# Performance work log

Measured on AMD Instinct MI355X. Metric: run time of the kernel, lower is better.

The kernel has to match this reference:

```python
import jax, jax.numpy as jnp
import numpy as np

D = 256; NH = 8; HD = 32; DFF = 1024; NL = 4; NPT = 4
SHAPES = [(100, 100), (50, 50), (25, 25), (13, 13)]
LEN_V = sum(h * w for h, w in SHAPES)  # 13294
BS = 16; LQ = 300


def _ln(x, g, b):
    m = jnp.mean(x, -1, keepdims=True)
    v = jnp.var(x, -1, keepdims=True)
    return (x - m) * jax.lax.rsqrt(v + 1e-5) * g + b


def _bilinear(v, loc, H, W):
    # v: [bs, nh, H*W, hd]; loc: [bs, Lq, nh, P, 2] normalized [0,1]
    # matches F.grid_sample(bilinear, align_corners=False, padding_mode='zeros')
    bs, Lq, nh, P, _ = loc.shape
    x = loc[..., 0] * W - 0.5
    y = loc[..., 1] * H - 0.5
    x0 = jnp.floor(x); y0 = jnp.floor(y)
    dx = x - x0; dy = y - y0
    x0 = x0.astype(jnp.int32); y0 = y0.astype(jnp.int32)
    out = jnp.zeros((bs, Lq, nh, P, v.shape[-1]), v.dtype)
    for ix, iy, w in ((x0, y0, (1 - dx) * (1 - dy)),
                      (x0 + 1, y0, dx * (1 - dy)),
                      (x0, y0 + 1, (1 - dx) * dy),
                      (x0 + 1, y0 + 1, dx * dy)):
        valid = (ix >= 0) & (ix < W) & (iy >= 0) & (iy < H)
        idx = jnp.clip(iy, 0, H - 1) * W + jnp.clip(ix, 0, W - 1)  # [bs,Lq,nh,P]
        idx = jnp.transpose(idx, (0, 2, 1, 3)).reshape(bs, nh, Lq * P, 1)
        g = jnp.take_along_axis(v, idx, axis=2).reshape(bs, nh, Lq, P, -1)
        g = jnp.transpose(g, (0, 2, 1, 3, 4))  # [bs,Lq,nh,P,hd]
        out = out + g * jnp.where(valid, w, jnp.zeros_like(w))[..., None]
    return out


def reference(tgt, reference_points, memory, Wq, bq, Wk, bk, Wv, bv, Wo, bo,
              Wvp, bvp, Wso, bso, Waw, baw, Wop, bop, W1, bf1, W2, bf2,
              ln1_g, ln1_b, ln2_g, ln2_b, ln3_g, ln3_b):
    bs, Lq, _ = tgt.shape
    # ---- self attention (query_pos_embed=None, attn_mask=None) ----
    qh = (tgt @ Wq + bq).reshape(bs, Lq, NH, HD)
    kh = (tgt @ Wk + bk).reshape(bs, Lq, NH, HD)
    vh = (tgt @ Wv + bv).reshape(bs, Lq, NH, HD)
    scores = jnp.einsum('bqhd,bkhd->bhqk', qh, kh) * np.float32(1.0 / np.sqrt(HD))
    attn = jax.nn.softmax(scores, -1)
    sa = jnp.einsum('bhqk,bkhd->bqhd', attn, vh).reshape(bs, Lq, D) @ Wo + bo
    t = _ln(tgt + sa, ln1_g, ln1_b)
    # ---- PP multi-scale deformable cross attention ----
    val = (memory @ Wvp + bvp).reshape(bs, LEN_V, NH, HD)
    val = jnp.transpose(val, (0, 2, 1, 3))  # [bs, nh, Lv, hd]
    off = (t @ Wso + bso).reshape(bs, Lq, NH, NL, NPT, 2)
    aw = jax.nn.softmax((t @ Waw + baw).reshape(bs, Lq, NH, NL * NPT), -1)
    aw = aw.reshape(bs, Lq, NH, NL, NPT)
    rp = reference_points  # [bs, Lq, NL, 4] -> (cx, cy, w, h) branch
    loc = rp[:, :, None, :, None, :2] + off / NPT * rp[:, :, None, :, None, 2:] * 0.5
    start = 0
    ca = jnp.zeros((bs, Lq, NH, HD), t.dtype)
    for l, (H, W) in enumerate(SHAPES):
        v_l = val[:, :, start:start + H * W]
        sampled = _bilinear(v_l, loc[:, :, :, l], H, W)  # [bs,Lq,nh,P,hd]
        ca = ca + jnp.einsum('bqhpd,bqhp->bqhd', sampled, aw[:, :, :, l])
        start += H * W
    ca = ca.reshape(bs, Lq, D) @ Wop + bop
    t = _ln(t + ca, ln2_g, ln2_b)
    # ---- FFN ----
    ff = jax.nn.relu(t @ W1 + bf1) @ W2 + bf2
    return _ln(t + ff, ln3_g, ln3_b)


def setup_inputs() -> dict:
    ks = iter(jax.random.split(jax.random.key(0), 64))
    inp = {}
    inp['tgt'] = jax.random.normal(next(ks), (BS, LQ, D), jnp.float32)
    inp['reference_points'] = jax.random.uniform(next(ks), (BS, LQ, NL, 4), jnp.float32)
    inp['memory'] = jax.random.normal(next(ks), (BS, LEN_V, D), jnp.float32)
    for name, sh in [('Wq', (D, D)), ('Wk', (D, D)), ('Wv', (D, D)), ('Wo', (D, D)),
                     ('Wvp', (D, D)), ('Wso', (D, NH * NL * NPT * 2)),
                     ('Waw', (D, NH * NL * NPT)), ('Wop', (D, D)),
                     ('W1', (D, DFF)), ('W2', (DFF, D))]:
        inp[name] = jax.random.normal(next(ks), sh, jnp.float32) * 0.02
    for name, dim in [('bq', D), ('bk', D), ('bv', D), ('bo', D), ('bvp', D),
                      ('bso', NH * NL * NPT * 2), ('baw', NH * NL * NPT),
                      ('bop', D), ('bf1', DFF), ('bf2', D)]:
        inp[name] = jnp.zeros((dim,), jnp.float32)
    for g, b in [('ln1_g', 'ln1_b'), ('ln2_g', 'ln2_b'), ('ln3_g', 'ln3_b')]:
        inp[g] = jnp.ones((D,), jnp.float32)
        inp[b] = jnp.zeros((D,), jnp.float32)
    return inp
```

## Files before the change

### kernel.cpp

```cpp
#include <hip/hip_runtime.h>
#include <hip/hip_bf16.h>
#include <cstddef>

#define D_    256
#define NH_   8
#define HD_   32
#define LQ_   300
#define BS_   16
#define LENV_ 13294
#define DFF_  1024
#define NROWS (BS_*LQ_)
#define VROWS (BS_*LENV_)

typedef __attribute__((ext_vector_type(8))) short short8;
typedef __attribute__((ext_vector_type(4))) float f32x4;
typedef unsigned int u32;

__device__ __forceinline__ short f2bf(float x) {
    unsigned u = __float_as_uint(x);
    u += 0x7fff + ((u >> 16) & 1);
    return (short)(u >> 16);
}
__device__ __forceinline__ unsigned pack_bf2(float lo, float hi) {
    return (unsigned)(unsigned short)f2bf(lo) | ((unsigned)(unsigned short)f2bf(hi) << 16);
}
__device__ __forceinline__ float bf2f(short s) {
    return __uint_as_float((unsigned)(unsigned short)s << 16);
}

__global__ __launch_bounds__(256) void prep_all(
    const float* __restrict__ Wq, const float* __restrict__ Wk,
    const float* __restrict__ Wv, const float* __restrict__ Wo,
    const float* __restrict__ Wvp, const float* __restrict__ Wso,
    const float* __restrict__ Waw, const float* __restrict__ Wop,
    const float* __restrict__ W1, const float* __restrict__ W2,
    const float* __restrict__ bqp, const float* __restrict__ bkp,
    const float* __restrict__ bvp, const float* __restrict__ bsop,
    const float* __restrict__ bawp,
    short* __restrict__ Wqkvt, short* __restrict__ Wot,
    short* __restrict__ Wvpt, short* __restrict__ Wsoawt,
    short* __restrict__ Wopt, short* __restrict__ W1t,
    short* __restrict__ W2t, float* __restrict__ bqkv,
    float* __restrict__ bsoaw)
{
    const int blk = blockIdx.x, tid = threadIdx.x;
    if (blk < 1792) {
        const int seg = blk >> 8;
        const int e = ((blk & 255) << 8) | tid;
        const int n = e >> 8, k = e & 255;
        const float* src; short* dst;
        switch (seg) {
            case 0: src = Wq;  dst = Wqkvt;          break;
            case 1: src = Wk;  dst = Wqkvt + 65536;  break;
            case 2: src = Wv;  dst = Wqkvt + 131072; break;
            case 3: src = Wo;  dst = Wot;            break;
            case 4: src = Wvp; dst = Wvpt;           break;
            case 5: src = Wso; dst = Wsoawt;         break;
            default: src = Wop; dst = Wopt;          break;
        }
        dst[e] = f2bf(src[(size_t)k * 256 + n]);
    } else if (blk < 1920) {
        const int e = ((blk - 1792) << 8) | tid;
        const int n = e >> 8, k = e & 255;
        Wsoawt[65536 + e] = f2bf(Waw[(size_t)k * 128 + n]);
    } else if (blk < 2048) {
        const int e = ((blk - 1920) << 8) | tid;
        Wsoawt[98304 + e] = 0;
    } else if (blk < 3072) {
        const int e = ((blk - 2048) << 8) | tid;
        const int n = e >> 8, k = e & 255;
        W1t[e] = f2bf(W1[(size_t)k * 1024 + n]);
    } else if (blk < 4096) {
        const int e = ((blk - 3072) << 8) | tid;
        const int n = e / 1024, k = e % 1024;
        W2t[e] = f2bf(W2[(size_t)k * 256 + n]);
    } else {
        const int e = ((blk - 4096) << 8) | tid;
        if (e < 768)
            bqkv[e] = (e < 256) ? bqp[e] : (e < 512) ? bkp[e - 256] : bvp[e - 512];
        else if (e < 1280) {
            const int f = e - 768;
            bsoaw[f] = (f < 256) ? bsop[f] : (f < 384) ? bawp[f - 256] : 0.f;
        }
    }
}

template<int ACT, int OUT_BF16, int STACKED>
__global__ __launch_bounds__(256) void mfma_gemm(
    const float* __restrict__ A, const short* __restrict__ Wt,
    const float* __restrict__ bias, void* __restrict__ Cout,
    int M, int N, int K)
{
    __shared__ short Alds[2][64 * 40];
    __shared__ short Blds[2][256 * 40];
    const int tid  = threadIdx.x;
    const int lane = tid & 63;
    const int wn   = tid >> 6;
    const int m0   = blockIdx.x * 64;
    const int nb   = blockIdx.y;
    const int srow = tid >> 2;
    const int schk = tid & 3;

    const int  arow = m0 + srow;
    const bool aok  = (arow < M);
    const float* aptr = &A[(size_t)(aok ? arow : 0) * K + schk * 8];
    const short* bptr = &Wt[(size_t)(nb * 256 + srow) * K + schk * 8];

    f32x4 acc[4][4] = {};
    float4 ra0, ra1;
    short8 rb0, rb1, rb2, rb3;

    ra0 = make_float4(0.f, 0.f, 0.f, 0.f); ra1 = ra0;
    if (aok) { ra0 = *(const float4*)(aptr); ra1 = *(const float4*)(aptr + 4); }
    rb0 = *(const short8*)(bptr);
    rb1 = *(const short8*)(bptr + (size_t)64 * K);
    rb2 = *(const short8*)(bptr + (size_t)128 * K);
    rb3 = *(const short8*)(bptr + (size_t)192 * K);
    {
        short8 s;
        s[0] = f2bf(ra0.x); s[1] = f2bf(ra0.y); s[2] = f2bf(ra0.z); s[3] = f2bf(ra0.w);
        s[4] = f2bf(ra1.x); s[5] = f2bf(ra1.y); s[6] = f2bf(ra1.z); s[7] = f2bf(ra1.w);
        *(short8*)&Alds[0][srow * 40 + schk * 8] = s;
        *(short8*)&Blds[0][(srow +   0) * 40 + schk * 8] = rb0;
        *(short8*)&Blds[0][(srow +  64) * 40 + schk * 8] = rb1;
        *(short8*)&Blds[0][(srow + 128) * 40 + schk * 8] = rb2;
        *(short8*)&Blds[0][(srow + 192) * 40 + schk * 8] = rb3;
    }
    __syncthreads();

    const int lg = lane >> 4;
    const int lr = lane & 15;
    int buf = 0;

    for (int k0 = 32; k0 < K; k0 += 32) {
        ra0 = make_float4(0.f, 0.f, 0.f, 0.f); ra1 = ra0;
        if (aok) { ra0 = *(const float4*)(aptr + k0); ra1 = *(const float4*)(aptr + k0 + 4); }
        rb0 = *(const short8*)(bptr + k0);
        rb1 = *(const short8*)(bptr + k0 + (size_t)64 * K);
        rb2 = *(const short8*)(bptr + k0 + (size_t)128 * K);
        rb3 = *(const short8*)(bptr + k0 + (size_t)192 * K);

        {
            short8 a[4], b[4];
            #pragma unroll
            for (int mr = 0; mr < 4; ++mr)
                a[mr] = *(const short8*)&Alds[buf][(mr * 16 + lr) * 40 + lg * 8];
            #pragma unroll
            for (int nr = 0; nr < 4; ++nr)
                b[nr] = *(const short8*)&Blds[buf][(wn * 64 + nr * 16 + lr) * 40 + lg * 8];
            #pragma unroll
            for (int mr = 0; mr < 4; ++mr)
                #pragma unroll
                for (int nr = 0; nr < 4; ++nr)
                    acc[mr][nr] = __builtin_amdgcn_mfma_f32_16x16x32_bf16(
                        a[mr], b[nr], acc[mr][nr], 0, 0, 0);
        }

        {
            short8 s;
            s[0] = f2bf(ra0.x); s[1] = f2bf(ra0.y); s[2] = f2bf(ra0.z); s[3] = f2bf(ra0.w);
            s[4] = f2bf(ra1.x); s[5] = f2bf(ra1.y); s[6] = f2bf(ra1.z); s[7] = f2bf(ra1.w);
            const int ob = buf ^ 1;
            *(short8*)&Alds[ob][srow * 40 + schk * 8] = s;
            *(short8*)&Blds[ob][(srow +   0) * 40 + schk * 8] = rb0;
            *(short8*)&Blds[ob][(srow +  64) * 40 + schk * 8] = rb1;
            *(short8*)&Blds[ob][(srow + 128) * 40 + schk * 8] = rb2;
            *(short8*)&Blds[ob][(srow + 192) * 40 + schk * 8] = rb3;
        }
        __syncthreads();
        buf ^= 1;
    }

    {
        short8 a[4], b[4];
        #pragma unroll
        for (int mr = 0; mr < 4; ++mr)
            a[mr] = *(const short8*)&Alds[buf][(mr * 16 + lr) * 40 + lg * 8];
        #pragma unroll
        for (int nr = 0; nr < 4; ++nr)
            b[nr] = *(const short8*)&Blds[buf][(wn * 64 + nr * 16 + lr) * 40 + lg * 8];
        #pragma unroll
        for (int mr = 0; mr < 4; ++mr)
            #pragma unroll
            for (int nr = 0; nr < 4; ++nr)
                acc[mr][nr] = __builtin_amdgcn_mfma_f32_16x16x32_bf16(
                    a[mr], b[nr], acc[mr][nr], 0, 0, 0);
    }

    if (STACKED) {
        float* Cb = (float*)Cout + (size_t)nb * M * 256;
        const float* bb = bias + nb * 256;
        #pragma unroll
        for (int mr = 0; mr < 4; ++mr)
            #pragma unroll
            for (int r = 0; r < 4; ++r) {
                const int row = m0 + mr * 16 + lg * 4 + r;
                if (row >= M) continue;
                #pragma unroll
                for (int nr = 0; nr < 4; ++nr) {
                    const int col = wn * 64 + nr * 16 + lr;
                    Cb[(size_t)row * 256 + col] = acc[mr][nr][r] + bb[col];
                }
            }
    } else {
        #pragma unroll
        for (int mr = 0; mr < 4; ++mr)
            #pragma unroll
            for (int r = 0; r < 4; ++r) {
                const int row = m0 + mr * 16 + lg * 4 + r;
                if (row >= M) continue;
                #pragma unroll
                for (int nr = 0; nr < 4; ++nr) {
                    const int col = nb * 256 + wn * 64 + nr * 16 + lr;
                    float v = acc[mr][nr][r] + bias[col];
                    if (ACT) v = fmaxf(v, 0.f);
                    if (OUT_BF16) ((short*)Cout)[(size_t)row * N + col] = f2bf(v);
                    else          ((float*)Cout)[(size_t)row * N + col] = v;
                }
            }
    }
}

__global__ __launch_bounds__(256, 2) void vp_gemm(
    const float* __restrict__ A, const short* __restrict__ Wt,
    const float* __restrict__ bias, short* __restrict__ C)
{
    __shared__ float Alds[2][32 * 256];
    __shared__ short Cst[32 * 256];
    const int tid  = threadIdx.x;
    const int lane = tid & 63;
    const int w    = tid >> 6;
    const int lr   = lane & 15;
    const int lg   = lane >> 4;

    short8 bf[4][8];
    #pragma unroll
    for (int nr = 0; nr < 4; ++nr) {
        const short* wp = &Wt[(size_t)(w * 64 + nr * 16 + lr) * 256 + lg * 8];
        #pragma unroll
        for (int kc = 0; kc < 8; ++kc)
            bf[nr][kc] = *(const short8*)(wp + kc * 32);
    }
    float bs[4];
    #pragma unroll
    for (int nr = 0; nr < 4; ++nr) bs[nr] = bias[w * 64 + nr * 16 + lr];

    const int NT = VROWS / 32;
    const int NB = 512;
    int t = blockIdx.x;
    int buf = 0;

    #define VP_STAGE(BUFI, TILE)                                               \
        {                                                                      \
            _Pragma("unroll")                                                  \
            for (int j = 0; j < 8; ++j) {                                      \
                const int r = w * 8 + j;                                       \
                const int grow = (TILE) * 32 + r;                              \
                const int c16 = ((((lane >> 1) ^ (r & 7)) << 1) | (lane & 1)); \
                const float* src = A + (size_t)grow * 256 + c16 * 4;           \
                __builtin_amdgcn_global_load_lds(                              \
                    (const __attribute__((address_space(1))) u32*)src,         \
                    (__attribute__((address_space(3))) u32*)&Alds[BUFI][r*256],\
                    16, 0, 0);                                                 \
            }                                                                  \
        }

    VP_STAGE(0, t);
    __syncthreads();

    while (true) {
        const int t2 = t + NB;
        if (t2 < NT) VP_STAGE(buf ^ 1, t2);

        f32x4 acc[2][4] = {};
        #pragma unroll
        for (int kc = 0; kc < 8; ++kc) {
            short8 a[2];
            #pragma unroll
            for (int mr = 0; mr < 2; ++mr) {
                const int row = mr * 16 + lr;
                const int c32 = (kc * 4 + lg) ^ (row & 7);
                const float* p = &Alds[buf][row * 256 + c32 * 8];
                float4 x = *(const float4*)(p);
                float4 y = *(const float4*)(p + 4);
                short8 s;
                s[0] = f2bf(x.x); s[1] = f2bf(x.y); s[2] = f2bf(x.z); s[3] = f2bf(x.w);
                s[4] = f2bf(y.x); s[5] = f2bf(y.y); s[6] = f2bf(y.z); s[7] = f2bf(y.w);
                a[mr] = s;
            }
            #pragma unroll
            for (int mr = 0; mr < 2; ++mr)
                #pragma unroll
                for (int nr = 0; nr < 4; ++nr)
                    acc[mr][nr] = __builtin_amdgcn_mfma_f32_16x16x32_bf16(
                        a[mr], bf[nr][kc], acc[mr][nr], 0, 0, 0);
        }

        #pragma unroll
        for (int mr = 0; mr < 2; ++mr)
            #pragma unroll
            for (int r4 = 0; r4 < 4; ++r4)
                #pragma unroll
                for (int nr = 0; nr < 4; ++nr)
                    Cst[(mr * 16 + lg * 4 + r4) * 256 + w * 64 + nr * 16 + lr] =
                        f2bf(acc[mr][nr][r4] + bs[nr]);
        __syncthreads();

        {
            const size_t base = (size_t)t * 32 * 256;
            #pragma unroll
            for (int j = 0; j < 4; ++j) {
                const int chunk = j * 256 + tid;
                *(short8*)&C[base + (size_t)chunk * 8] =
                    *(const short8*)&Cst[chunk * 8];
            }
        }
        __syncthreads();
        buf ^= 1;
        if (t2 >= NT) break;
        t = t2;
    }
    #undef VP_STAGE
}

__global__ __launch_bounds__(256) void attn_fused(
    const float* __restrict__ qh, const float* __restrict__ kh,
    const float* __restrict__ vh, float* __restrict__ sa)
{
    __shared__ short Klds[304 * 40];
    __shared__ short Vtlds[32 * 328];
    const int bh = blockIdx.x, b = bh / NH_, h = bh % NH_;
    const int tid = threadIdx.x;

    for (int idx = tid; idx < 304 * 4; idx += 256) {
        const int key = idx >> 2, dc = idx & 3;
        short8 s = {};
        if (key < LQ_) {
            const float* kp = &kh[((size_t)(b * LQ_ + key)) * D_ + h * HD_ + dc * 8];
            float4 a0 = *reinterpret_cast<const float4*>(kp);
            float4 a1 = *reinterpret_cast<const float4*>(kp + 4);
            s[0] = f2bf(a0.x); s[1] = f2bf(a0.y); s[2] = f2bf(a0.z); s[3] = f2bf(a0.w);
            s[4] = f2bf(a1.x); s[5] = f2bf(a1.y); s[6] = f2bf(a1.z); s[7] = f2bf(a1.w);
        }
        *reinterpret_cast<short8*>(&Klds[key * 40 + dc * 8]) = s;
    }
    for (int idx = tid; idx < LQ_ * 8; idx += 256) {
        const int key = idx >> 3, dc = idx & 7;
        const float4 v4 = *reinterpret_cast<const float4*>(
            &vh[((size_t)(b * LQ_ + key)) * D_ + h * HD_ + dc * 4]);
        Vtlds[(dc * 4 + 0) * 328 + key] = f2bf(v4.x);
        Vtlds[(dc * 4 + 1) * 328 + key] = f2bf(v4.y);
        Vtlds[(dc * 4 + 2) * 328 + key] = f2bf(v4.z);
        Vtlds[(dc * 4 + 3) * 328 + key] = f2bf(v4.w);
    }
    for (int idx = tid; idx < 32 * 20; idx += 256) {
        const int d = idx / 20, kk = idx % 20;
        Vtlds[d * 328 + 300 + kk] = 0;
    }
    __syncthreads();

    const int lane = tid & 63;
    const int wid  = tid >> 6;
    const int g    = lane >> 4;
    const int qc   = lane & 15;
    const int y    = blockIdx.y;
    const int qt_end = (y == 0) ? 10 : 19;

    for (int qt = y * 10 + wid; qt < qt_end; qt += 4) {
        const int q0 = qt * 16;
        short8 qf;
        {
            const int q = min(q0 + qc, LQ_ - 1);
            const float* qp = &qh[((size_t)(b * LQ_ + q)) * D_ + h * HD_ + g * 8];
            float4 a0 = *reinterpret_cast<const float4*>(qp);
            float4 a1 = *reinterpret_cast<const float4*>(qp + 4);
            const float sc = 0.17677669529663687f;
            qf[0] = f2bf(a0.x * sc); qf[1] = f2bf(a0.y * sc);
            qf[2] = f2bf(a0.z * sc); qf[3] = f2bf(a0.w * sc);
            qf[4] = f2bf(a1.x * sc); qf[5] = f2bf(a1.y * sc);
            qf[6] = f2bf(a1.z * sc); qf[7] = f2bf(a1.w * sc);
        }
        f32x4 s[19];
        #pragma unroll
        for (int kt = 0; kt < 19; ++kt) {
            short8 kf = *reinterpret_cast<const short8*>(&Klds[(kt * 16 + qc) * 40 + g * 8]);
            f32x4 z = {};
            s[kt] = __builtin_amdgcn_mfma_f32_16x16x32_bf16(kf, qf, z, 0, 0, 0);
        }
        if (g == 3) { s[18][0] = -1e30f; s[18][1] = -1e30f; s[18][2] = -1e30f; s[18][3] = -1e30f; }

        float m = -1e30f;
        #pragma unroll
        for (int kt = 0; kt < 19; ++kt)
            #pragma unroll
            for (int r = 0; r < 4; ++r) m = fmaxf(m, s[kt][r]);
        m = fmaxf(m, __shfl_xor(m, 16));
        m = fmaxf(m, __shfl_xor(m, 32));
        float sum = 0.f;
        #pragma unroll
        for (int kt = 0; kt < 19; ++kt)
            #pragma unroll
            for (int r = 0; r < 4; ++r) {
                float e = __expf(s[kt][r] - m);
                s[kt][r] = e; sum += e;
            }
        sum += __shfl_xor(sum, 16);
        sum += __shfl_xor(sum, 32);
        const float inv = 1.f / sum;

        unsigned pb0[20], pb1[20];
        #pragma unroll
        for (int kt = 0; kt < 19; ++kt) {
            pb0[kt] = pack_bf2(s[kt][0] * inv, s[kt][1] * inv);
            pb1[kt] = pack_bf2(s[kt][2] * inv, s[kt][3] * inv);
        }
        pb0[19] = 0; pb1[19] = 0;

        f32x4 acc0 = {}, acc1 = {};
        const int src0 = ((g & 1) << 5) + qc;
        const int src1 = src0 + 16;
        const bool hi = (g >> 1);
        #pragma unroll
        for (int c = 0; c < 10; ++c) {
            short8 va0 = *reinterpret_cast<const short8*>(&Vtlds[qc * 328 + c * 32 + g * 8]);
            short8 va1 = *reinterpret_cast<const short8*>(&Vtlds[(qc + 16) * 328 + c * 32 + g * 8]);
            int x0a = __shfl((int)pb0[2 * c], src0), x0b = __shfl((int)pb0[2 * c + 1], src0);
            int x1a = __shfl((int)pb1[2 * c], src0), x1b = __shfl((int)pb1[2 * c + 1], src0);
            int x2a = __shfl((int)pb0[2 * c], src1), x2b = __shfl((int)pb0[2 * c + 1], src1);
            int x3a = __shfl((int)pb1[2 * c], src1), x3b = __shfl((int)pb1[2 * c + 1], src1);
            union { int u[4]; short8 s8; } pb;
            pb.u[0] = hi ? x0b : x0a;
            pb.u[1] = hi ? x1b : x1a;
            pb.u[2] = hi ? x2b : x2a;
            pb.u[3] = hi ? x3b : x3a;
            acc0 = __builtin_amdgcn_mfma_f32_16x16x32_bf16(va0, pb.s8, acc0, 0, 0, 0);
            acc1 = __builtin_amdgcn_mfma_f32_16x16x32_bf16(va1, pb.s8, acc1, 0, 0, 0);
        }

        if (q0 + qc < LQ_) {
            float* op = &sa[((size_t)(b * LQ_ + q0 + qc)) * D_ + h * HD_ + 4 * g];
            *reinterpret_cast<float4*>(op)      = make_float4(acc0[0], acc0[1], acc0[2], acc0[3]);
            *reinterpret_cast<float4*>(op + 16) = make_float4(acc1[0], acc1[1], acc1[2], acc1[3]);
        }
    }
}

__global__ __launch_bounds__(64) void ln_kernel(
    const float* __restrict__ x, const float* __restrict__ res,
    const float* __restrict__ g, const float* __restrict__ bb,
    float* __restrict__ out)
{
    const size_t row = blockIdx.x;
    const int lane = threadIdx.x;
    const float* xp = x + row * D_;
    const float* rp = res + row * D_;
    float v[4], s = 0.f, s2 = 0.f;
    #pragma unroll
    for (int j = 0; j < 4; ++j) {
        v[j] = xp[lane + j * 64] + rp[lane + j * 64];
        s += v[j]; s2 += v[j] * v[j];
    }
    #pragma unroll
    for (int o = 32; o; o >>= 1) { s += __shfl_xor(s, o); s2 += __shfl_xor(s2, o); }
    const float mean = s * (1.f / D_);
    const float var  = s2 * (1.f / D_) - mean * mean;
    const float inv  = rsqrtf(var + 1e-5f);
    #pragma unroll
    for (int j = 0; j < 4; ++j) {
        int c = lane + j * 64;
        out[row * D_ + c] = (v[j] - mean) * inv * g[c] + bb[c];
    }
}

__global__ __launch_bounds__(256) void deform_kernel(
    const __hip_bfloat16* __restrict__ val, const float* __restrict__ off,
    const float* __restrict__ aw, const float* __restrict__ rp,
    float* __restrict__ ca)
{
    const int i = blockIdx.x * 256 + threadIdx.x;
    if (i >= NROWS * NH_ * 4) return;
    const int dq = i & 3;
    const int h  = (i >> 2) & 7;
    const int bq = i >> 5;
    const int b  = bq / LQ_;

    const int Hs[4] = {100, 50, 25, 13};
    const int st[4] = {0, 10000, 12500, 13125};

    const float* rpp  = rp  + (size_t)bq * 16;
    const float* offp = off + (size_t)bq * 256 + h * 32;
    const float* awp  = aw  + (size_t)bq * 256 + h * 16;
    const short* vb   = (const short*)val + ((size_t)b * LENV_) * D_ + h * HD_ + dq * 8;

    float wv[16], wmax = -1e30f, wsum = 0.f;
    #pragma unroll
    for (int j = 0; j < 16; ++j) { wv[j] = awp[j]; wmax = fmaxf(wmax, wv[j]); }
    #pragma unroll
    for (int j = 0; j < 16; ++j) { wv[j] = __expf(wv[j] - wmax); wsum += wv[j]; }
    const float winv = 1.f / wsum;

    float acc[8] = {};
    #pragma unroll
    for (int l = 0; l < 4; ++l) {
        const float cx = rpp[l * 4 + 0], cy = rpp[l * 4 + 1];
        const float sw = rpp[l * 4 + 2], sh = rpp[l * 4 + 3];
        const int H = Hs[l], W = Hs[l];
        const int base = st[l];
        #pragma unroll
        for (int p = 0; p < 4; ++p) {
            const float ox = offp[l * 8 + p * 2 + 0];
            const float oy = offp[l * 8 + p * 2 + 1];
            const float x = (cx + ox * 0.125f * sw) * W - 0.5f;
            const float y = (cy + oy * 0.125f * sh) * H - 0.5f;
            const float x0f = floorf(x), y0f = floorf(y);
            const float dx = x - x0f, dy = y - y0f;
            const int x0 = (int)x0f, y0 = (int)y0f;
            const float a = wv[l * 4 + p] * winv;

            float tp[8] = {};
            #pragma unroll
            for (int t = 0; t < 4; ++t) {
                const int ix = x0 + (t & 1);
                const int iy = y0 + (t >> 1);
                const float wx = (t & 1) ? dx : (1.f - dx);
                const float wy = (t >> 1) ? dy : (1.f - dy);
                const bool valid = (ix >= 0) & (ix < W) & (iy >= 0) & (iy < H);
                const int cxi = min(max(ix, 0), W - 1);
                const int cyi = min(max(iy, 0), H - 1);
                const float w = valid ? wx * wy : 0.f;
                const short8 u = *reinterpret_cast<const short8*>(
                    &vb[(size_t)(base + cyi * W + cxi) * D_]);
                #pragma unroll
                for (int k = 0; k < 8; ++k)
                    tp[k] = fmaf(w, bf2f(u[k]), tp[k]);
            }
            #pragma unroll
            for (int k = 0; k < 8; ++k)
                acc[k] = fmaf(a, tp[k], acc[k]);
        }
    }
    float* op = &ca[(size_t)i * 8];
    *reinterpret_cast<float4*>(op)     = make_float4(acc[0], acc[1], acc[2], acc[3]);
    *reinterpret_cast<float4*>(op + 4) = make_float4(acc[4], acc[5], acc[6], acc[7]);
}

extern "C" void kernel_launch(void* const* d_in, const int* in_sizes, int n_in,
                              void* d_out, int out_size, void* d_ws, size_t ws_size,
                              hipStream_t stream)
{
    const float* tgt    = (const float*)d_in[0];
    const float* refpts = (const float*)d_in[1];
    const float* memory = (const float*)d_in[2];
    const float* Wq  = (const float*)d_in[3];
    const float* Wk  = (const float*)d_in[4];
    const float* Wv  = (const float*)d_in[5];
    const float* Wo  = (const float*)d_in[6];
    const float* Wvp = (const float*)d_in[7];
    const float* Wso = (const float*)d_in[8];
    const float* Waw = (const float*)d_in[9];
    const float* Wop = (const float*)d_in[10];
    const float* W1  = (const float*)d_in[11];
    const float* W2  = (const float*)d_in[12];
    const float* bq  = (const float*)d_in[13];
    const float* bk  = (const float*)d_in[14];
    const float* bv  = (const float*)d_in[15];
    const float* bo  = (const float*)d_in[16];
    const float* bvp = (const float*)d_in[17];
    const float* bso = (const float*)d_in[18];
    const float* baw = (const float*)d_in[19];
    const float* bop = (const float*)d_in[20];
    const float* bf1 = (const float*)d_in[21];
    const float* bf2 = (const float*)d_in[22];
    const float* ln1g = (const float*)d_in[23];
    const float* ln1b = (const float*)d_in[24];
    const float* ln2g = (const float*)d_in[25];
    const float* ln2b = (const float*)d_in[26];
    const float* ln3g = (const float*)d_in[27];
    const float* ln3b = (const float*)d_in[28];
    float* out = (float*)d_out;

    const size_t SZ = (size_t)NROWS * D_;
    float* ws = (float*)d_ws;
    float* reg1 = ws;
    float* reg2 = ws + SZ;
    float* reg3 = ws + 2 * SZ;
    float* t    = ws + 3 * SZ;
    float* t2   = ws + 4 * SZ;
    float* big  = ws + 5 * SZ;

    float* qh = reg1;
    float* kh = reg2;
    float* vh = reg3;
    float* sa_heads = t2;
    float* sa_o = big;
    __hip_bfloat16* val = (__hip_bfloat16*)big;
    float* off_raw = reg2;
    float* aw_raw  = reg3;
    float* ca_heads = reg1;
    float* ca_o = reg2;
    float* ff1 = big;
    float* ff2 = reg1;

    char* wtbase = (char*)d_ws + 5 * SZ * sizeof(float) + (size_t)VROWS * D_ * 2;
    short* Wqkvt  = (short*)wtbase;
    short* Wot    = Wqkvt  + 196608;
    short* Wvpt   = Wot    + 65536;
    short* Wsoawt = Wvpt   + 65536;
    short* Wopt   = Wsoawt + 131072;
    short* W1t    = Wopt   + 65536;
    short* W2t    = W1t    + 262144;
    float* bqkv   = (float*)(W2t + 262144);
    float* bsoaw  = bqkv + 768;

    const dim3 blk(256);

    prep_all<<<dim3(4101), blk, 0, stream>>>(
        Wq, Wk, Wv, Wo, Wvp, Wso, Waw, Wop, W1, W2,
        bq, bk, bv, bso, baw,
        Wqkvt, Wot, Wvpt, Wsoawt, Wopt, W1t, W2t, bqkv, bsoaw);

    mfma_gemm<0,0,1><<<dim3(75, 3), blk, 0, stream>>>(tgt, Wqkvt, bqkv, reg1, NROWS, 256, D_);

    attn_fused<<<dim3(BS_ * NH_, 2), blk, 0, stream>>>(qh, kh, vh, sa_heads);

    mfma_gemm<0,0,0><<<dim3(75, 1), blk, 0, stream>>>(sa_heads, Wot, bo, sa_o, NROWS, 256, D_);
    ln_kernel<<<dim3(NROWS), dim3(64), 0, stream>>>(sa_o, tgt, ln1g, ln1b, t);

    vp_gemm<<<dim3(512), blk, 0, stream>>>(memory, Wvpt, bvp, (short*)val);

    mfma_gemm<0,0,1><<<dim3(75, 2), blk, 0, stream>>>(t, Wsoawt, bsoaw, reg2, NROWS, 256, D_);

    deform_kernel<<<dim3((NROWS * NH_ * 4 + 255) / 256), blk, 0, stream>>>(
        val, off_raw, aw_raw, refpts, ca_heads);

    mfma_gemm<0,0,0><<<dim3(75, 1), blk, 0, stream>>>(ca_heads, Wopt, bop, ca_o, NROWS, 256, D_);
    ln_kernel<<<dim3(NROWS), dim3(64), 0, stream>>>(ca_o, t, ln2g, ln2b, t2);

    mfma_gemm<1,0,0><<<dim3(75, 4), blk, 0, stream>>>(t2, W1t, bf1, ff1, NROWS, DFF_, D_);
    mfma_gemm<0,0,0><<<dim3(75, 1), blk, 0, stream>>>(ff1, W2t, bf2, ff2, NROWS, 256, DFF_);
    ln_kernel<<<dim3(NROWS), dim3(64), 0, stream>>>(ff2, t2, ln3g, ln3b, out);
}
```

Before: 226.6 us.

## Fuse residual+LayerNorm into N=256 GEMM epilogues and deepen vp_gemm prefetch

Adds a FUSE_LN epilogue to the MFMA GEMM. When N is 256 a block owns whole rows, so bias, residual add and LayerNorm are computed in-register, with a shuffle plus LDS cross-wave reduction. This removes the three separate ln_kernel launches and their intermediate round trips through global memory. Separately, vp_gemm's pipeline is restructured to keep two tiles in flight, using explicit vmcnt waits and raw s_barrier in place of __syncthreads. That gives more load overlap but relies on exact hand-counted wait values.

```diff
diff --git a/kernel.cpp b/kernel.cpp
--- a/kernel.cpp
+++ b/kernel.cpp
@@ -85,11 +85,13 @@
     }
 }
 
-template<int ACT, int OUT_BF16, int STACKED>
+template<int ACT, int OUT_BF16, int STACKED, int FUSE_LN>
 __global__ __launch_bounds__(256) void mfma_gemm(
     const float* __restrict__ A, const short* __restrict__ Wt,
     const float* __restrict__ bias, void* __restrict__ Cout,
-    int M, int N, int K)
+    int M, int N, int K,
+    const float* __restrict__ resid, const float* __restrict__ lng,
+    const float* __restrict__ lnb)
 {
     __shared__ short Alds[2][64 * 40];
     __shared__ short Blds[2][256 * 40];
@@ -187,6 +189,68 @@
                     a[mr], b[nr], acc[mr][nr], 0, 0, 0);
     }
 
+    if (FUSE_LN) {
+        __shared__ float RedS[4][64];
+        __shared__ float RedS2[4][64];
+        float psum[4][4] = {};
+        float psq[4][4]  = {};
+        #pragma unroll
+        for (int mr = 0; mr < 4; ++mr)
+            #pragma unroll
+            for (int r4 = 0; r4 < 4; ++r4) {
+                const int row = m0 + mr * 16 + lg * 4 + r4;
+                #pragma unroll
+                for (int nr = 0; nr < 4; ++nr) {
+                    const int col = wn * 64 + nr * 16 + lr;
+                    float x = acc[mr][nr][r4] + bias[col]
+                            + resid[(size_t)row * 256 + col];
+                    acc[mr][nr][r4] = x;
+                    psum[mr][r4] += x;
+                    psq[mr][r4]  += x * x;
+                }
+            }
+        #pragma unroll
+        for (int o = 1; o < 16; o <<= 1)
+            #pragma unroll
+            for (int mr = 0; mr < 4; ++mr)
+                #pragma unroll
+                for (int r4 = 0; r4 < 4; ++r4) {
+                    psum[mr][r4] += __shfl_xor(psum[mr][r4], o);
+                    psq[mr][r4]  += __shfl_xor(psq[mr][r4], o);
+                }
+        if (lr == 0) {
+            #pragma unroll
+            for (int mr = 0; mr < 4; ++mr)
+                #pragma unroll
+                for (int r4 = 0; r4 < 4; ++r4) {
+                    const int lrow = mr * 16 + lg * 4 + r4;
+                    RedS[wn][lrow]  = psum[mr][r4];
+                    RedS2[wn][lrow] = psq[mr][r4];
+                }
+        }
+        __syncthreads();
+        float* outp = (float*)Cout;
+        #pragma unroll
+        for (int mr = 0; mr < 4; ++mr)
+            #pragma unroll
+            for (int r4 = 0; r4 < 4; ++r4) {
+                const int lrow = mr * 16 + lg * 4 + r4;
+                const int row  = m0 + lrow;
+                const float s  = RedS[0][lrow] + RedS[1][lrow] + RedS[2][lrow] + RedS[3][lrow];
+                const float s2 = RedS2[0][lrow] + RedS2[1][lrow] + RedS2[2][lrow] + RedS2[3][lrow];
+                const float mean = s * (1.f / 256.f);
+                const float var  = s2 * (1.f / 256.f) - mean * mean;
+                const float inv  = rsqrtf(var + 1e-5f);
+                #pragma unroll
+                for (int nr = 0; nr < 4; ++nr) {
+                    const int col = wn * 64 + nr * 16 + lr;
+                    outp[(size_t)row * 256 + col] =
+                        (acc[mr][nr][r4] - mean) * inv * lng[col] + lnb[col];
+                }
+            }
+        return;
+    }
+
     if (STACKED) {
         float* Cb = (float*)Cout + (size_t)nb * M * 256;
         const float* bb = bias + nb * 256;
@@ -247,8 +311,6 @@
 
     const int NT = VROWS / 32;
     const int NB = 512;
-    int t = blockIdx.x;
-    int buf = 0;
 
     #define VP_STAGE(BUFI, TILE)                                               \
         {                                                                      \
@@ -265,13 +327,19 @@
             }                                                                  \
         }
 
+    int t  = blockIdx.x;
+    int t2 = t + NB;
+    bool has2 = (t2 < NT);
+    int buf = 0;
+
     VP_STAGE(0, t);
-    __syncthreads();
+    if (has2) VP_STAGE(1, t2);
+    if (has2) { asm volatile("s_waitcnt vmcnt(8)" ::: "memory"); }
+    else      { asm volatile("s_waitcnt vmcnt(0)" ::: "memory"); }
+    __builtin_amdgcn_sched_barrier(0);
+    __builtin_amdgcn_s_barrier();
 
     while (true) {
-        const int t2 = t + NB;
-        if (t2 < NT) VP_STAGE(buf ^ 1, t2);
-
         f32x4 acc[2][4] = {};
         #pragma unroll
         for (int kc = 0; kc < 8; ++kc) {
@@ -304,7 +372,14 @@
                 for (int nr = 0; nr < 4; ++nr)
                     Cst[(mr * 16 + lg * 4 + r4) * 256 + w * 64 + nr * 16 + lr] =
                         f2bf(acc[mr][nr][r4] + bs[nr]);
-        __syncthreads();
+
+        asm volatile("s_waitcnt lgkmcnt(0)" ::: "memory");
+        __builtin_amdgcn_sched_barrier(0);
+        __builtin_amdgcn_s_barrier();
+
+        const int t3 = t2 + NB;
+        const bool has3 = has2 && (t3 < NT);
+        if (has3) VP_STAGE(buf, t3);
 
         {
             const size_t base = (size_t)t * 32 * 256;
@@ -315,10 +390,17 @@
                     *(const short8*)&Cst[chunk * 8];
             }
         }
-        __syncthreads();
+
+        if (has2) {
+            if (has3) { asm volatile("s_waitcnt vmcnt(12)" ::: "memory"); }
+            else      { asm volatile("s_waitcnt vmcnt(4)"  ::: "memory"); }
+        }
+        __builtin_amdgcn_sched_barrier(0);
+        __builtin_amdgcn_s_barrier();
+
+        if (!has2) break;
         buf ^= 1;
-        if (t2 >= NT) break;
-        t = t2;
+        t = t2; t2 = t3; has2 = has3;
     }
     #undef VP_STAGE
 }
@@ -442,33 +524,6 @@
             *reinterpret_cast<float4*>(op)      = make_float4(acc0[0], acc0[1], acc0[2], acc0[3]);
             *reinterpret_cast<float4*>(op + 16) = make_float4(acc1[0], acc1[1], acc1[2], acc1[3]);
         }
-    }
-}
-
-__global__ __launch_bounds__(64) void ln_kernel(
-    const float* __restrict__ x, const float* __restrict__ res,
-    const float* __restrict__ g, const float* __restrict__ bb,
-    float* __restrict__ out)
-{
-    const size_t row = blockIdx.x;
-    const int lane = threadIdx.x;
-    const float* xp = x + row * D_;
-    const float* rp = res + row * D_;
-    float v[4], s = 0.f, s2 = 0.f;
-    #pragma unroll
-    for (int j = 0; j < 4; ++j) {
-        v[j] = xp[lane + j * 64] + rp[lane + j * 64];
-        s += v[j]; s2 += v[j] * v[j];
-    }
-    #pragma unroll
-    for (int o = 32; o; o >>= 1) { s += __shfl_xor(s, o); s2 += __shfl_xor(s2, o); }
-    const float mean = s * (1.f / D_);
-    const float var  = s2 * (1.f / D_) - mean * mean;
-    const float inv  = rsqrtf(var + 1e-5f);
-    #pragma unroll
-    for (int j = 0; j < 4; ++j) {
-        int c = lane + j * 64;
-        out[row * D_ + c] = (v[j] - mean) * inv * g[c] + bb[c];
     }
 }
 
@@ -592,14 +647,11 @@
     float* kh = reg2;
     float* vh = reg3;
     float* sa_heads = t2;
-    float* sa_o = big;
     __hip_bfloat16* val = (__hip_bfloat16*)big;
     float* off_raw = reg2;
     float* aw_raw  = reg3;
     float* ca_heads = reg1;
-    float* ca_o = reg2;
     float* ff1 = big;
-    float* ff2 = reg1;
 
     char* wtbase = (char*)d_ws + 5 * SZ * sizeof(float) + (size_t)VROWS * D_ * 2;
     short* Wqkvt  = (short*)wtbase;
@@ -619,24 +671,27 @@
         bq, bk, bv, bso, baw,
         Wqkvt, Wot, Wvpt, Wsoawt, Wopt, W1t, W2t, bqkv, bsoaw);
 
-    mfma_gemm<0,0,1><<<dim3(75, 3), blk, 0, stream>>>(tgt, Wqkvt, bqkv, reg1, NROWS, 256, D_);
+    mfma_gemm<0,0,1,0><<<dim3(75, 3), blk, 0, stream>>>(
+        tgt, Wqkvt, bqkv, reg1, NROWS, 256, D_, nullptr, nullptr, nullptr);
 
     attn_fused<<<dim3(BS_ * NH_, 2), blk, 0, stream>>>(qh, kh, vh, sa_heads);
 
-    mfma_gemm<0,0,0><<<dim3(75, 1), blk, 0, stream>>>(sa_heads, Wot, bo, sa_o, NROWS, 256, D_);
-    ln_kernel<<<dim3(NROWS), dim3(64), 0, stream>>>(sa_o, tgt, ln1g, ln1b, t);
+    mfma_gemm<0,0,0,1><<<dim3(75, 1), blk, 0, stream>>>(
+        sa_heads, Wot, bo, t, NROWS, 256, D_, tgt, ln1g, ln1b);
 
     vp_gemm<<<dim3(512), blk, 0, stream>>>(memory, Wvpt, bvp, (short*)val);
 
-    mfma_gemm<0,0,1><<<dim3(75, 2), blk, 0, stream>>>(t, Wsoawt, bsoaw, reg2, NROWS, 256, D_);
+    mfma_gemm<0,0,1,0><<<dim3(75, 2), blk, 0, stream>>>(
+        t, Wsoawt, bsoaw, reg2, NROWS, 256, D_, nullptr, nullptr, nullptr);
 
     deform_kernel<<<dim3((NROWS * NH_ * 4 + 255) / 256), blk, 0, stream>>>(
         val, off_raw, aw_raw, refpts, ca_heads);
 
-    mfma_gemm<0,0,0><<<dim3(75, 1), blk, 0, stream>>>(ca_heads, Wopt, bop, ca_o, NROWS, 256, D_);
-    ln_kernel<<<dim3(NROWS), dim3(64), 0, stream>>>(ca_o, t, ln2g, ln2b, t2);
-
-    mfma_gemm<1,0,0><<<dim3(75, 4), blk, 0, stream>>>(t2, W1t, bf1, ff1, NROWS, DFF_, D_);
-    mfma_gemm<0,0,0><<<dim3(75, 1), blk, 0, stream>>>(ff1, W2t, bf2, ff2, NROWS, 256, DFF_);
-    ln_kernel<<<dim3(NROWS), dim3(64), 0, stream>>>(ff2, t2, ln3g, ln3b, out);
-}
+    mfma_gemm<0,0,0,1><<<dim3(75, 1), blk, 0, stream>>>(
+        ca_heads, Wopt, bop, t2, NROWS, 256, D_, t, ln2g, ln2b);
+
+    mfma_gemm<1,0,0,0><<<dim3(75, 4), blk, 0, stream>>>(
+        t2, W1t, bf1, ff1, NROWS, DFF_, D_, nullptr, nullptr, nullptr);
+    mfma_gemm<0,0,0,1><<<dim3(75, 1), blk, 0, stream>>>(
+        ff1, W2t, bf2, out, NROWS, 256, DFF_, t2, ln3g, ln3b);
+}
```

Measured after the change: 223.6 us. Within noise of the previous version (-1.3%).
